# Kernel optimization log

Measured on AMD Instinct MI355X. Metric: run time of the kernel, lower is better.

The kernel has to match this reference:

```python
import jax, jax.numpy as jnp
import numpy as np

B, S, IN, H, NH = 8, 1024, 512, 512, 8
HD = H // NH
EPS = 1e-5

def _ln(x, g, b):
    m = jnp.mean(x, axis=-1, keepdims=True)
    v = jnp.mean((x - m) ** 2, axis=-1, keepdims=True)
    return (x - m) * jax.lax.rsqrt(v + EPS) * g + b

def setup_inputs() -> dict:
    key = jax.random.key(0)
    ks = iter(jax.random.split(key, 32))
    r = lambda shape: jax.random.normal(next(ks), shape, dtype=jnp.float32) * 0.02
    return {
        "x": jax.random.normal(next(ks), (B, S, IN), dtype=jnp.float32),
        "in_proj_w": r((H, IN)), "in_proj_b": jnp.zeros((H,), jnp.float32),
        "attn_qkv_w": r((3 * H, H)), "attn_qkv_b": jnp.zeros((3 * H,), jnp.float32),
        "attn_out_w": r((H, H)), "attn_out_b": jnp.zeros((H,), jnp.float32),
        "ltc_w1": r((H, 2 * H)), "ltc_b1": jnp.zeros((H,), jnp.float32),
        "ltc_w2": r((H, H)), "ltc_b2": jnp.zeros((H,), jnp.float32),
        "time_w": r((H, H)), "time_b": jnp.zeros((H,), jnp.float32),
        "g_w": r((H, H)), "g_b": jnp.zeros((H,), jnp.float32),
        "hn_w": r((H, H)), "hn_b": jnp.zeros((H,), jnp.float32),
        "norm1_g": jnp.ones((H,), jnp.float32), "norm1_b": jnp.zeros((H,), jnp.float32),
        "norm2_g": jnp.ones((H,), jnp.float32), "norm2_b": jnp.zeros((H,), jnp.float32),
        "out_w": r((IN, H)), "out_b": jnp.zeros((IN,), jnp.float32),
    }

def reference(x, in_proj_w, in_proj_b, attn_qkv_w, attn_qkv_b, attn_out_w, attn_out_b,
              ltc_w1, ltc_b1, ltc_w2, ltc_b2, time_w, time_b, g_w, g_b, hn_w, hn_b,
              norm1_g, norm1_b, norm2_g, norm2_b, out_w, out_b):
    b, s, _ = x.shape
    # input projection
    h = x @ in_proj_w.T + in_proj_b                      # [B,S,H]
    # multi-head self-attention (no mask, eval: no dropout)
    qkv = h @ attn_qkv_w.T + attn_qkv_b                  # [B,S,3H]
    q, k, v = jnp.split(qkv, 3, axis=-1)
    q = q.reshape(b, s, NH, HD)
    k = k.reshape(b, s, NH, HD)
    v = v.reshape(b, s, NH, HD)
    scores = jnp.einsum("bqhd,bkhd->bhqk", q, k) / jnp.sqrt(jnp.float32(HD))
    attn = jax.nn.softmax(scores, axis=-1)
    ctx = jnp.einsum("bhqk,bkhd->bqhd", attn, v).reshape(b, s, H)
    h_att = ctx @ attn_out_w.T + attn_out_b
    h_att = _ln(h + h_att, norm1_g, norm1_b)             # [B,S,H]
    # LTC recurrence over time via scan
    times = jnp.arange(s, dtype=jnp.float32)             # default times, same per batch
    def step(state, inp):
        xt, tt = inp                                      # [B,H], scalar
        combined = jnp.concatenate([xt, state], axis=-1)  # [B,2H]
        feats = jnp.tanh(combined @ ltc_w1.T + ltc_b1) @ ltc_w2.T + ltc_b2
        f_t = jax.nn.sigmoid(feats @ time_w.T + time_b)
        g_x = feats @ g_w.T + g_b
        h_x = feats @ hn_w.T + hn_b
        gate = jax.nn.sigmoid(-f_t * tt)
        h_new = gate * g_x + (1.0 - gate) * h_x
        return h_new, h_new
    init = jnp.zeros((b, H), x.dtype)
    _, outs = jax.lax.scan(step, init, (h_att.transpose(1, 0, 2), times))
    outs = outs.transpose(1, 0, 2)                        # [B,S,H]
    outs = _ln(outs + h_att, norm2_g, norm2_b)
    return outs @ out_w.T + out_b                         # [B,S,IN]
```

## Files before the change

kernel.cpp:

```cpp
#include <hip/hip_runtime.h>
#include <math.h>

#define HALF _Float16
typedef _Float16 half8 __attribute__((ext_vector_type(8)));
typedef float floatx4 __attribute__((ext_vector_type(4)));

#define SPIN_MAX (1 << 14)

__global__ __launch_bounds__(256) void k_cast(const float* __restrict__ s, HALF* __restrict__ d, int n) {
    int i = blockIdx.x * 256 + threadIdx.x;
    if (i < n) d[i] = (HALF)s[i];
}

__global__ __launch_bounds__(256) void k_cast_slice(const float* __restrict__ s, HALF* __restrict__ d, int off) {
    int i = blockIdx.x * 256 + threadIdx.x;
    int r = i >> 9, c = i & 511;
    d[i] = (HALF)s[r * 1024 + off + c];
}

__global__ __launch_bounds__(256) void k_transpose_cast(const float* __restrict__ s, HALF* __restrict__ d) {
    int i = blockIdx.x * 256 + threadIdx.x;
    int r = i >> 9, c = i & 511;
    d[c * 512 + r] = (HALF)s[i];
}

__global__ __launch_bounds__(256) void k_fuse_bias(const float* __restrict__ b2,
    const float* __restrict__ tw, const float* __restrict__ tb,
    const float* __restrict__ gw, const float* __restrict__ gb,
    const float* __restrict__ hw, const float* __restrict__ hb,
    float* __restrict__ bcat) {
    int i = blockIdx.x * 256 + threadIdx.x;
    if (i >= 1536) return;
    int j = i >> 9, n = i & 511;
    const float* W  = (j == 0) ? tw : (j == 1 ? gw : hw);
    const float* bb = (j == 0) ? tb : (j == 1 ? gb : hb);
    float s = bb[n];
    for (int k = 0; k < 512; ++k) s += b2[k] * W[n * 512 + k];
    bcat[i] = s;
}

__global__ __launch_bounds__(256) void k_reorderA(const float* __restrict__ in, float* __restrict__ out) {
    int i = blockIdx.x * 256 + threadIdx.x;
    int nl = i & 7, m = (i >> 3) & 7, blk = (i >> 6) & 63, t = i >> 12;
    out[i] = in[((long long)(m << 10 | t)) * 512 + blk * 8 + nl];
}

__global__ __launch_bounds__(256)
void k_gemm(const HALF* __restrict__ A, int lda, long long sAz,
            const HALF* __restrict__ Bw, int ldb, long long sBz,
            float* __restrict__ Cf, HALF* __restrict__ Ch, int ldc, long long sCz,
            const float* __restrict__ bias, float alpha,
            int M, int N, int K)
{
    __shared__ HALF As[64][72];
    __shared__ HALF Ws[64][72];
    const int tid = threadIdx.x;
    const int bx = blockIdx.x, by = blockIdx.y, z = blockIdx.z;
    A  += (long long)z * sAz;
    Bw += (long long)z * sBz;
    const long long coff = (long long)z * sCz;
    const int wave = tid >> 6, lane = tid & 63;
    const int wrow = (wave >> 1) * 32, wcol = (wave & 1) * 32;
    const int frow = lane & 15, fquad = lane >> 4;
    const int srow = tid >> 3, sch = (tid & 7) * 8;
    floatx4 acc[2][2] = {};
    for (int k0 = 0; k0 < K; k0 += 64) {
        uint4 a0 = *(const uint4*)(A + (long long)(by * 64 + srow) * lda + k0 + sch);
        uint4 a1 = *(const uint4*)(A + (long long)(by * 64 + srow + 32) * lda + k0 + sch);
        uint4 b0 = *(const uint4*)(Bw + (long long)(bx * 64 + srow) * ldb + k0 + sch);
        uint4 b1 = *(const uint4*)(Bw + (long long)(bx * 64 + srow + 32) * ldb + k0 + sch);
        *(uint4*)&As[srow][sch] = a0;
        *(uint4*)&As[srow + 32][sch] = a1;
        *(uint4*)&Ws[srow][sch] = b0;
        *(uint4*)&Ws[srow + 32][sch] = b1;
        __syncthreads();
        #pragma unroll
        for (int ks = 0; ks < 64; ks += 32) {
            half8 fa0 = *(const half8*)&As[wrow + frow][ks + fquad * 8];
            half8 fa1 = *(const half8*)&As[wrow + 16 + frow][ks + fquad * 8];
            half8 fb0 = *(const half8*)&Ws[wcol + frow][ks + fquad * 8];
            half8 fb1 = *(const half8*)&Ws[wcol + 16 + frow][ks + fquad * 8];
            acc[0][0] = __builtin_amdgcn_mfma_f32_16x16x32_f16(fa0, fb0, acc[0][0], 0, 0, 0);
            acc[0][1] = __builtin_amdgcn_mfma_f32_16x16x32_f16(fa0, fb1, acc[0][1], 0, 0, 0);
            acc[1][0] = __builtin_amdgcn_mfma_f32_16x16x32_f16(fa1, fb0, acc[1][0], 0, 0, 0);
            acc[1][1] = __builtin_amdgcn_mfma_f32_16x16x32_f16(fa1, fb1, acc[1][1], 0, 0, 0);
        }
        __syncthreads();
    }
    const int crow = (lane >> 4) * 4, ccol = lane & 15;
    #pragma unroll
    for (int i = 0; i < 2; ++i)
        #pragma unroll
        for (int j = 0; j < 2; ++j) {
            int gn = bx * 64 + wcol + j * 16 + ccol;
            float bv = bias ? bias[gn] : 0.0f;
            #pragma unroll
            for (int r = 0; r < 4; ++r) {
                int gm = by * 64 + wrow + i * 16 + crow + r;
                float v = acc[i][j][r] * alpha + bv;
                long long idx = coff + (long long)gm * ldc + gn;
                if (Cf) Cf[idx] = v;
                if (Ch) Ch[idx] = (HALF)v;
            }
        }
}

__global__ __launch_bounds__(256) void k_qkv_split(const HALF* __restrict__ qkv,
    HALF* __restrict__ Q, HALF* __restrict__ Kt, HALF* __restrict__ VT) {
    long long i = (long long)blockIdx.x * 256 + threadIdx.x;
    int c = (int)(i & 511);
    long long sg = i >> 9;
    int b = (int)(sg >> 10), s = (int)(sg & 1023);
    int h = c >> 6, d = c & 63;
    const HALF* src = qkv + sg * 1536;
    long long bh = (long long)(b * 8 + h);
    long long qi = (bh * 1024 + s) * 64 + d;
    Q[qi]  = src[c];
    Kt[qi] = src[512 + c];
    VT[(bh * 64 + d) * 1024 + s] = src[1024 + c];
}

__global__ __launch_bounds__(256) void k_softmax(HALF* __restrict__ P) {
    long long row = (long long)blockIdx.x * 4 + (threadIdx.x >> 6);
    int lane = threadIdx.x & 63;
    uint4* p = (uint4*)(P + row * 1024);
    union { uint4 u; HALF h[8]; } u0, u1;
    u0.u = p[lane * 2]; u1.u = p[lane * 2 + 1];
    float f[16];
    #pragma unroll
    for (int i = 0; i < 8; ++i) { f[i] = (float)u0.h[i]; f[8 + i] = (float)u1.h[i]; }
    float mx = f[0];
    #pragma unroll
    for (int i = 1; i < 16; ++i) mx = fmaxf(mx, f[i]);
    #pragma unroll
    for (int o = 32; o > 0; o >>= 1) mx = fmaxf(mx, __shfl_xor(mx, o, 64));
    float sm = 0.f;
    #pragma unroll
    for (int i = 0; i < 16; ++i) { f[i] = __expf(f[i] - mx); sm += f[i]; }
    #pragma unroll
    for (int o = 32; o > 0; o >>= 1) sm += __shfl_xor(sm, o, 64);
    float r = 1.0f / sm;
    #pragma unroll
    for (int i = 0; i < 8; ++i) { u0.h[i] = (HALF)(f[i] * r); u1.h[i] = (HALF)(f[8 + i] * r); }
    p[lane * 2] = u0.u; p[lane * 2 + 1] = u1.u;
}

__global__ __launch_bounds__(256) void k_ln_add(const float* __restrict__ X, const float* __restrict__ Y,
    const float* __restrict__ g, const float* __restrict__ bb,
    float* __restrict__ o32, HALF* __restrict__ o16) {
    long long row = (long long)blockIdx.x * 4 + (threadIdx.x >> 6);
    int lane = threadIdx.x & 63;
    const float4* xp = (const float4*)(X + row * 512);
    const float4* yp = (const float4*)(Y + row * 512);
    float v[8];
    float s = 0.f, s2 = 0.f;
    #pragma unroll
    for (int i = 0; i < 2; ++i) {
        float4 a = xp[lane * 2 + i], c = yp[lane * 2 + i];
        float t0 = a.x + c.x, t1 = a.y + c.y, t2 = a.z + c.z, t3 = a.w + c.w;
        v[i * 4 + 0] = t0; v[i * 4 + 1] = t1; v[i * 4 + 2] = t2; v[i * 4 + 3] = t3;
        s += t0 + t1 + t2 + t3;
        s2 += t0 * t0 + t1 * t1 + t2 * t2 + t3 * t3;
    }
    #pragma unroll
    for (int o = 32; o > 0; o >>= 1) { s += __shfl_xor(s, o, 64); s2 += __shfl_xor(s2, o, 64); }
    float mean = s * (1.0f / 512.0f);
    float var = s2 * (1.0f / 512.0f) - mean * mean;
    float rstd = rsqrtf(var + 1e-5f);
    #pragma unroll
    for (int i = 0; i < 8; ++i) {
        int c = lane * 8 + i;
        float o = (v[i] - mean) * rstd * g[c] + bb[c];
        if (o32) o32[row * 512 + c] = o;
        if (o16) o16[row * 512 + c] = (HALF)o;
    }
}

__device__ __forceinline__ floatx4 mfma16(half8 a, half8 b, floatx4 c) {
    return __builtin_amdgcn_mfma_f32_16x16x32_f16(a, b, c, 0, 0, 0);
}
__device__ __forceinline__ unsigned long long pack2h_tag(float a, float b, unsigned tag) {
    union { unsigned short u; HALF h; } x0, x1;
    x0.h = (HALF)a; x1.h = (HALF)b;
    return (unsigned long long)x0.u | ((unsigned long long)x1.u << 16)
         | ((unsigned long long)tag << 48);
}
__device__ __forceinline__ float fast_tanh(float x) {
    float e = __expf(2.0f * x);
    return 1.0f - 2.0f / (e + 1.0f);
}

__global__ __launch_bounds__(256, 1)
void k_ltc_scan(const float* __restrict__ AscanR, const HALF* __restrict__ W1hg,
                const HALF* __restrict__ Wcatg, const float* __restrict__ bcat,
                unsigned long long* __restrict__ Sbuf, unsigned long long* __restrict__ Tbuf,
                float* __restrict__ outs)
{
    __shared__ unsigned int SLu[2][2176];
    const int tid = threadIdx.x;
    const int wv = tid >> 6, lane = tid & 63;
    const int blk = blockIdx.x * 4 + wv;
    const int n0 = blk * 8;
    const int c = lane & 15, q = lane >> 4;
    const int nW = n0 + (c & 7);
    const int kq = q * 8;
    const bool valid = (q < 2) && (c < 8);
    const int pidx = blk * 16 + c * 2 + q;
    const int i0 = tid * 8;

    for (int k = tid; k < 2176; k += 256) { SLu[0][k] = 0; SLu[1][k] = 0; }

    half8 aW1[16];
    half8 aWc[3][16];
    #pragma unroll
    for (int kb = 0; kb < 16; ++kb)
        aW1[kb] = *(const half8*)(W1hg + (long long)nW * 512 + kb * 32 + kq);
    #pragma unroll
    for (int j = 0; j < 3; ++j)
        #pragma unroll
        for (int kb = 0; kb < 16; ++kb)
            aWc[j][kb] = *(const half8*)(Wcatg + ((long long)j * 512 + nW) * 512 + kb * 32 + kq);
    floatx4 binit[3];
    #pragma unroll
    for (int j = 0; j < 3; ++j) {
        float4 bv = *(const float4*)(bcat + j * 512 + n0 + (q & 1) * 4);
        binit[j][0] = bv.x; binit[j][1] = bv.y; binit[j][2] = bv.z; binit[j][3] = bv.w;
    }

    auto stage_wait = [&](const unsigned long long* __restrict__ P, unsigned tag, int p) {
        unsigned long long v[8];
        #pragma unroll
        for (int k = 0; k < 8; ++k)
            v[k] = __hip_atomic_load(P + i0 + k, __ATOMIC_RELAXED, __HIP_MEMORY_SCOPE_SYSTEM);
        int spin = 0;
        for (;;) {
            bool ok = true;
            #pragma unroll
            for (int k = 0; k < 8; ++k) ok &= ((unsigned)(v[k] >> 48) == tag);
            if (ok || ++spin > SPIN_MAX) break;
            #pragma unroll
            for (int k = 0; k < 8; ++k)
                v[k] = __hip_atomic_load(P + i0 + k, __ATOMIC_RELAXED, __HIP_MEMORY_SCOPE_SYSTEM);
        }
        #pragma unroll
        for (int k = 0; k < 8; ++k) SLu[p][i0 + k] = (unsigned)v[k];
        __syncthreads();
    };

    for (int t = 0; t < 1024; ++t) {
        float4 aval = *(const float4*)(AscanR + (long long)t * 4096 + blk * 64 + (c & 7) * 8 + (q & 1) * 4);

        stage_wait(Sbuf, (unsigned)t, 0);
        const char* SLb0 = (const char*)SLu[0];

        floatx4 c1a = {0.f, 0.f, 0.f, 0.f}, c1b = {0.f, 0.f, 0.f, 0.f};
        #pragma unroll
        for (int kb = 0; kb < 16; kb += 2) {
            half8 b0 = *(const half8*)(SLb0 + kb * 512 + q * 128 + c * 16);
            half8 b1 = *(const half8*)(SLb0 + (kb + 1) * 512 + q * 128 + c * 16);
            c1a = mfma16(aW1[kb],     b0, c1a);
            c1b = mfma16(aW1[kb + 1], b1, c1b);
        }
        floatx4 c1 = c1a + c1b;
        float tv0 = fast_tanh(c1[0] + aval.x);
        float tv1 = fast_tanh(c1[1] + aval.y);
        float tv2 = fast_tanh(c1[2] + aval.z);
        float tv3 = fast_tanh(c1[3] + aval.w);
        if (valid) {
            __hip_atomic_store(Tbuf + pidx * 2,     pack2h_tag(tv0, tv1, (unsigned)(t + 1)),
                               __ATOMIC_RELAXED, __HIP_MEMORY_SCOPE_SYSTEM);
            __hip_atomic_store(Tbuf + pidx * 2 + 1, pack2h_tag(tv2, tv3, (unsigned)(t + 1)),
                               __ATOMIC_RELAXED, __HIP_MEMORY_SCOPE_SYSTEM);
        }

        stage_wait(Tbuf, (unsigned)(t + 1), 1);
        const char* SLb1 = (const char*)SLu[1];

        floatx4 c2_0 = binit[0], c2_1 = binit[1], c2_2 = binit[2];
        #pragma unroll
        for (int kb = 0; kb < 16; ++kb) {
            half8 bT = *(const half8*)(SLb1 + kb * 512 + q * 128 + c * 16);
            c2_0 = mfma16(aWc[0][kb], bT, c2_0);
            c2_1 = mfma16(aWc[1][kb], bT, c2_1);
            c2_2 = mfma16(aWc[2][kb], bT, c2_2);
        }
        float sn[4];
        const float tf = (float)t;
        #pragma unroll
        for (int r = 0; r < 4; ++r) {
            float f = 1.0f / (1.0f + __expf(-c2_0[r]));
            float gate = 1.0f / (1.0f + __expf(f * tf));
            sn[r] = gate * c2_1[r] + (1.0f - gate) * c2_2[r];
        }
        if (valid) {
            __hip_atomic_store(Sbuf + pidx * 2,     pack2h_tag(sn[0], sn[1], (unsigned)(t + 1)),
                               __ATOMIC_RELAXED, __HIP_MEMORY_SCOPE_SYSTEM);
            __hip_atomic_store(Sbuf + pidx * 2 + 1, pack2h_tag(sn[2], sn[3], (unsigned)(t + 1)),
                               __ATOMIC_RELAXED, __HIP_MEMORY_SCOPE_SYSTEM);
            float4 ov; ov.x = sn[0]; ov.y = sn[1]; ov.z = sn[2]; ov.w = sn[3];
            *(float4*)(outs + ((long long)(c << 10 | t)) * 512 + n0 + q * 4) = ov;
        }
    }
}

extern "C" void kernel_launch(void* const* d_in, const int* in_sizes, int n_in,
                              void* d_out, int out_size, void* d_ws, size_t ws_size,
                              hipStream_t stream) {
    (void)in_sizes; (void)n_in; (void)out_size; (void)ws_size;
    const float* x       = (const float*)d_in[0];
    const float* w_in_f  = (const float*)d_in[1];
    const float* b_in    = (const float*)d_in[2];
    const float* w_qkv_f = (const float*)d_in[3];
    const float* b_qkv   = (const float*)d_in[4];
    const float* w_ao_f  = (const float*)d_in[5];
    const float* b_ao    = (const float*)d_in[6];
    const float* w1_f    = (const float*)d_in[7];
    const float* b1      = (const float*)d_in[8];
    const float* w2_f    = (const float*)d_in[9];
    const float* b2      = (const float*)d_in[10];
    const float* tw_f    = (const float*)d_in[11];
    const float* tb      = (const float*)d_in[12];
    const float* gw_f    = (const float*)d_in[13];
    const float* gb      = (const float*)d_in[14];
    const float* hw_f    = (const float*)d_in[15];
    const float* hb      = (const float*)d_in[16];
    const float* n1g     = (const float*)d_in[17];
    const float* n1b     = (const float*)d_in[18];
    const float* n2g     = (const float*)d_in[19];
    const float* n2b     = (const float*)d_in[20];
    const float* w_out_f = (const float*)d_in[21];
    const float* b_out   = (const float*)d_in[22];
    float* out = (float*)d_out;

    char* p = (char*)d_ws;
    auto alloc = [&](size_t n) { char* r = p; p += (n + 255) & ~(size_t)255; return r; };
    HALF* w_in   = (HALF*)alloc(512 * 512 * 2);
    HALF* w_qkv  = (HALF*)alloc(1536 * 512 * 2);
    HALF* w_ao   = (HALF*)alloc(512 * 512 * 2);
    HALF* w_out  = (HALF*)alloc(512 * 512 * 2);
    HALF* w_time = (HALF*)alloc(512 * 512 * 2);
    HALF* w_g    = (HALF*)alloc(512 * 512 * 2);
    HALF* w_hn   = (HALF*)alloc(512 * 512 * 2);
    HALF* W2T    = (HALF*)alloc(512 * 512 * 2);
    HALF* W1x    = (HALF*)alloc(512 * 512 * 2);
    HALF* W1h    = (HALF*)alloc(512 * 512 * 2);
    HALF* Wcat   = (HALF*)alloc(3 * 512 * 512 * 2);
    float* bcat  = (float*)alloc(3 * 512 * 4 + 64);
    HALF* xb     = (HALF*)alloc(8192ll * 512 * 2);
    float* h32   = (float*)alloc(8192ll * 512 * 4);
    HALF* h16    = (HALF*)alloc(8192ll * 512 * 2);
    HALF* qkv16  = (HALF*)alloc(8192ll * 1536 * 2);
    HALF* Q16    = (HALF*)alloc(8192ll * 512 * 2);
    HALF* K16    = (HALF*)alloc(8192ll * 512 * 2);
    HALF* VT16   = (HALF*)alloc(8192ll * 512 * 2);
    HALF* P16    = (HALF*)alloc(8ll * 1024 * 1024 * 2);
    unsigned long long* Sbuf = (unsigned long long*)alloc(16384 + 256);
    unsigned long long* Tbuf = (unsigned long long*)alloc(16384 + 256);

    HALF*  ctx16      = xb;
    float* attnproj32 = (float*)qkv16;
    float* hatt32     = (float*)P16;
    HALF*  hatt16     = VT16;
    float* Ascan32    = h32;
    float* AscanR     = (float*)K16;
    float* outs32     = (float*)qkv16;
    HALF*  y16        = h16;

    hipMemsetAsync(Sbuf, 0, (16384 + 256) * 2, stream);

    k_cast<<<1024, 256, 0, stream>>>(w_in_f, w_in, 262144);
    k_cast<<<3072, 256, 0, stream>>>(w_qkv_f, w_qkv, 786432);
    k_cast<<<1024, 256, 0, stream>>>(w_ao_f, w_ao, 262144);
    k_cast<<<1024, 256, 0, stream>>>(w_out_f, w_out, 262144);
    k_cast<<<1024, 256, 0, stream>>>(tw_f, w_time, 262144);
    k_cast<<<1024, 256, 0, stream>>>(gw_f, w_g, 262144);
    k_cast<<<1024, 256, 0, stream>>>(hw_f, w_hn, 262144);
    k_cast<<<16384, 256, 0, stream>>>(x, xb, 4194304);
    k_transpose_cast<<<1024, 256, 0, stream>>>(w2_f, W2T);
    k_cast_slice<<<1024, 256, 0, stream>>>(w1_f, W1x, 0);
    k_cast_slice<<<1024, 256, 0, stream>>>(w1_f, W1h, 512);
    k_fuse_bias<<<6, 256, 0, stream>>>(b2, tw_f, tb, gw_f, gb, hw_f, hb, bcat);

    dim3 g88(8, 8, 1);
    k_gemm<<<g88, 256, 0, stream>>>(w_time, 512, 0, W2T, 512, 0, nullptr, Wcat,          512, 0, nullptr, 1.0f, 512, 512, 512);
    k_gemm<<<g88, 256, 0, stream>>>(w_g,    512, 0, W2T, 512, 0, nullptr, Wcat + 262144, 512, 0, nullptr, 1.0f, 512, 512, 512);
    k_gemm<<<g88, 256, 0, stream>>>(w_hn,   512, 0, W2T, 512, 0, nullptr, Wcat + 524288, 512, 0, nullptr, 1.0f, 512, 512, 512);

    dim3 gh(8, 128, 1);
    k_gemm<<<gh, 256, 0, stream>>>(xb, 512, 0, w_in, 512, 0, h32, h16, 512, 0, b_in, 1.0f, 8192, 512, 512);
    dim3 gq(24, 128, 1);
    k_gemm<<<gq, 256, 0, stream>>>(h16, 512, 0, w_qkv, 512, 0, nullptr, qkv16, 1536, 0, b_qkv, 1.0f, 8192, 1536, 512);
    k_qkv_split<<<16384, 256, 0, stream>>>(qkv16, Q16, K16, VT16);

    for (int c = 0; c < 8; ++c) {
        dim3 gs(16, 16, 8);
        k_gemm<<<gs, 256, 0, stream>>>(Q16 + c * 524288, 64, 65536, K16 + c * 524288, 64, 65536,
                                       nullptr, P16, 1024, 1048576, nullptr, 0.125f, 1024, 1024, 64);
        k_softmax<<<2048, 256, 0, stream>>>(P16);
        dim3 gc(1, 16, 8);
        k_gemm<<<gc, 256, 0, stream>>>(P16, 1024, 1048576, VT16 + c * 524288, 1024, 65536,
                                       nullptr, ctx16 + (long long)c * 524288, 512, 64, nullptr, 1.0f, 1024, 64, 1024);
    }

    k_gemm<<<gh, 256, 0, stream>>>(ctx16, 512, 0, w_ao, 512, 0, attnproj32, nullptr, 512, 0, b_ao, 1.0f, 8192, 512, 512);
    k_ln_add<<<2048, 256, 0, stream>>>(h32, attnproj32, n1g, n1b, hatt32, hatt16);

    k_gemm<<<gh, 256, 0, stream>>>(hatt16, 512, 0, W1x, 512, 0, Ascan32, nullptr, 512, 0, b1, 1.0f, 8192, 512, 512);
    k_reorderA<<<16384, 256, 0, stream>>>(Ascan32, AscanR);

    k_ltc_scan<<<16, 256, 0, stream>>>(AscanR, W1h, Wcat, bcat, Sbuf, Tbuf, outs32);

    k_ln_add<<<2048, 256, 0, stream>>>(outs32, hatt32, n2g, n2b, nullptr, y16);
    k_gemm<<<gh, 256, 0, stream>>>(y16, 512, 0, w_out, 512, 0, out, nullptr, 512, 0, b_out, 1.0f, 8192, 512, 512);
}
```

Before: 6.055 ms.

## Give each wave a private LDS state copy and drop block-wide barriers in scan

```diff
diff --git a/kernel.cpp b/kernel.cpp
--- a/kernel.cpp
+++ b/kernel.cpp
@@ -196,7 +196,7 @@
                 unsigned long long* __restrict__ Sbuf, unsigned long long* __restrict__ Tbuf,
                 float* __restrict__ outs)
 {
-    __shared__ unsigned int SLu[2][2176];
+    __shared__ unsigned int SLu[2][4][2176];
     const int tid = threadIdx.x;
     const int wv = tid >> 6, lane = tid & 63;
     const int blk = blockIdx.x * 4 + wv;
@@ -206,9 +206,8 @@
     const int kq = q * 8;
     const bool valid = (q < 2) && (c < 8);
     const int pidx = blk * 16 + c * 2 + q;
-    const int i0 = tid * 8;
-
-    for (int k = tid; k < 2176; k += 256) { SLu[0][k] = 0; SLu[1][k] = 0; }
+
+    for (int k = lane; k < 2176; k += 64) { SLu[0][wv][k] = 0; SLu[1][wv][k] = 0; }
 
     half8 aW1[16];
     half8 aWc[3][16];
@@ -226,32 +225,43 @@
         float4 bv = *(const float4*)(bcat + j * 512 + n0 + (q & 1) * 4);
         binit[j][0] = bv.x; binit[j][1] = bv.y; binit[j][2] = bv.z; binit[j][3] = bv.w;
     }
-
-    auto stage_wait = [&](const unsigned long long* __restrict__ P, unsigned tag, int p) {
-        unsigned long long v[8];
-        #pragma unroll
-        for (int k = 0; k < 8; ++k)
-            v[k] = __hip_atomic_load(P + i0 + k, __ATOMIC_RELAXED, __HIP_MEMORY_SCOPE_SYSTEM);
-        int spin = 0;
-        for (;;) {
-            bool ok = true;
+    #pragma unroll
+    for (int kb = 0; kb < 16; ++kb) asm volatile("" : "+v"(aW1[kb]));
+    #pragma unroll
+    for (int j = 0; j < 3; ++j)
+        #pragma unroll
+        for (int kb = 0; kb < 16; ++kb) asm volatile("" : "+v"(aWc[j][kb]));
+    #pragma unroll
+    for (int j = 0; j < 3; ++j) asm volatile("" : "+v"(binit[j]));
+
+    auto stage_wait = [&](const unsigned long long* __restrict__ P, unsigned tag, unsigned int* __restrict__ SL) {
+        #pragma unroll
+        for (int ch = 0; ch < 4; ++ch) {
+            const int base = lane + ch * 512;
+            unsigned long long v[8];
             #pragma unroll
-            for (int k = 0; k < 8; ++k) ok &= ((unsigned)(v[k] >> 48) == tag);
-            if (ok || ++spin > SPIN_MAX) break;
+            for (int j = 0; j < 8; ++j)
+                v[j] = __hip_atomic_load(P + base + 64 * j, __ATOMIC_RELAXED, __HIP_MEMORY_SCOPE_SYSTEM);
+            int spin = 0;
+            for (;;) {
+                bool ok = true;
+                #pragma unroll
+                for (int j = 0; j < 8; ++j) ok &= ((unsigned)(v[j] >> 48) == tag);
+                if (ok || ++spin > SPIN_MAX) break;
+                #pragma unroll
+                for (int j = 0; j < 8; ++j)
+                    v[j] = __hip_atomic_load(P + base + 64 * j, __ATOMIC_RELAXED, __HIP_MEMORY_SCOPE_SYSTEM);
+            }
             #pragma unroll
-            for (int k = 0; k < 8; ++k)
-                v[k] = __hip_atomic_load(P + i0 + k, __ATOMIC_RELAXED, __HIP_MEMORY_SCOPE_SYSTEM);
-        }
-        #pragma unroll
-        for (int k = 0; k < 8; ++k) SLu[p][i0 + k] = (unsigned)v[k];
-        __syncthreads();
+            for (int j = 0; j < 8; ++j) SL[base + 64 * j] = (unsigned)v[j];
+        }
     };
 
     for (int t = 0; t < 1024; ++t) {
         float4 aval = *(const float4*)(AscanR + (long long)t * 4096 + blk * 64 + (c & 7) * 8 + (q & 1) * 4);
 
-        stage_wait(Sbuf, (unsigned)t, 0);
-        const char* SLb0 = (const char*)SLu[0];
+        stage_wait(Sbuf, (unsigned)t, SLu[0][wv]);
+        const char* SLb0 = (const char*)SLu[0][wv];
 
         floatx4 c1a = {0.f, 0.f, 0.f, 0.f}, c1b = {0.f, 0.f, 0.f, 0.f};
         #pragma unroll
@@ -273,8 +283,8 @@
                                __ATOMIC_RELAXED, __HIP_MEMORY_SCOPE_SYSTEM);
         }
 
-        stage_wait(Tbuf, (unsigned)(t + 1), 1);
-        const char* SLb1 = (const char*)SLu[1];
+        stage_wait(Tbuf, (unsigned)(t + 1), SLu[1][wv]);
+        const char* SLb1 = (const char*)SLu[1][wv];
 
         floatx4 c2_0 = binit[0], c2_1 = binit[1], c2_2 = binit[2];
         #pragma unroll
```

New measurement: 8.722 ms. +44.0%, slower.

## Halve LTC scan workgroups by giving each wave 16 output columns

Applied to the files above, without the earlier changes.

```diff
diff --git a/kernel.cpp b/kernel.cpp
--- a/kernel.cpp
+++ b/kernel.cpp
@@ -199,13 +199,11 @@
     __shared__ unsigned int SLu[2][2176];
     const int tid = threadIdx.x;
     const int wv = tid >> 6, lane = tid & 63;
-    const int blk = blockIdx.x * 4 + wv;
-    const int n0 = blk * 8;
+    const int slice = blockIdx.x * 4 + wv;
+    const int n0 = slice * 16;
     const int c = lane & 15, q = lane >> 4;
-    const int nW = n0 + (c & 7);
-    const int kq = q * 8;
-    const bool valid = (q < 2) && (c < 8);
-    const int pidx = blk * 16 + c * 2 + q;
+    const bool valid = (c < 8);
+    const int w0 = slice * 64 + c * 8 + q * 2;
     const int i0 = tid * 8;
 
     for (int k = tid; k < 2176; k += 256) { SLu[0][k] = 0; SLu[1][k] = 0; }
@@ -214,16 +212,16 @@
     half8 aWc[3][16];
     #pragma unroll
     for (int kb = 0; kb < 16; ++kb)
-        aW1[kb] = *(const half8*)(W1hg + (long long)nW * 512 + kb * 32 + kq);
+        aW1[kb] = *(const half8*)(W1hg + (long long)(n0 + c) * 512 + kb * 32 + q * 8);
     #pragma unroll
     for (int j = 0; j < 3; ++j)
         #pragma unroll
         for (int kb = 0; kb < 16; ++kb)
-            aWc[j][kb] = *(const half8*)(Wcatg + ((long long)j * 512 + nW) * 512 + kb * 32 + kq);
+            aWc[j][kb] = *(const half8*)(Wcatg + ((long long)j * 512 + n0 + c) * 512 + kb * 32 + q * 8);
     floatx4 binit[3];
     #pragma unroll
     for (int j = 0; j < 3; ++j) {
-        float4 bv = *(const float4*)(bcat + j * 512 + n0 + (q & 1) * 4);
+        float4 bv = *(const float4*)(bcat + j * 512 + n0 + q * 4);
         binit[j][0] = bv.x; binit[j][1] = bv.y; binit[j][2] = bv.z; binit[j][3] = bv.w;
     }
 
@@ -248,7 +246,8 @@
     };
 
     for (int t = 0; t < 1024; ++t) {
-        float4 aval = *(const float4*)(AscanR + (long long)t * 4096 + blk * 64 + (c & 7) * 8 + (q & 1) * 4);
+        float4 aval = *(const float4*)(AscanR + (long long)t * 4096
+                                       + slice * 128 + (q >> 1) * 64 + c * 8 + (q & 1) * 4);
 
         stage_wait(Sbuf, (unsigned)t, 0);
         const char* SLb0 = (const char*)SLu[0];
@@ -256,8 +255,8 @@
         floatx4 c1a = {0.f, 0.f, 0.f, 0.f}, c1b = {0.f, 0.f, 0.f, 0.f};
         #pragma unroll
         for (int kb = 0; kb < 16; kb += 2) {
-            half8 b0 = *(const half8*)(SLb0 + kb * 512 + q * 128 + c * 16);
-            half8 b1 = *(const half8*)(SLb0 + (kb + 1) * 512 + q * 128 + c * 16);
+            half8 b0 = *(const half8*)(SLb0 + kb * 512 + (q >> 1) * 256 + c * 32 + (q & 1) * 16);
+            half8 b1 = *(const half8*)(SLb0 + (kb + 1) * 512 + (q >> 1) * 256 + c * 32 + (q & 1) * 16);
             c1a = mfma16(aW1[kb],     b0, c1a);
             c1b = mfma16(aW1[kb + 1], b1, c1b);
         }
@@ -267,9 +266,9 @@
         float tv2 = fast_tanh(c1[2] + aval.z);
         float tv3 = fast_tanh(c1[3] + aval.w);
         if (valid) {
-            __hip_atomic_store(Tbuf + pidx * 2,     pack2h_tag(tv0, tv1, (unsigned)(t + 1)),
+            __hip_atomic_store(Tbuf + w0,     pack2h_tag(tv0, tv1, (unsigned)(t + 1)),
                                __ATOMIC_RELAXED, __HIP_MEMORY_SCOPE_SYSTEM);
-            __hip_atomic_store(Tbuf + pidx * 2 + 1, pack2h_tag(tv2, tv3, (unsigned)(t + 1)),
+            __hip_atomic_store(Tbuf + w0 + 1, pack2h_tag(tv2, tv3, (unsigned)(t + 1)),
                                __ATOMIC_RELAXED, __HIP_MEMORY_SCOPE_SYSTEM);
         }
 
@@ -279,7 +278,7 @@
         floatx4 c2_0 = binit[0], c2_1 = binit[1], c2_2 = binit[2];
         #pragma unroll
         for (int kb = 0; kb < 16; ++kb) {
-            half8 bT = *(const half8*)(SLb1 + kb * 512 + q * 128 + c * 16);
+            half8 bT = *(const half8*)(SLb1 + kb * 512 + (q >> 1) * 256 + c * 32 + (q & 1) * 16);
             c2_0 = mfma16(aWc[0][kb], bT, c2_0);
             c2_1 = mfma16(aWc[1][kb], bT, c2_1);
             c2_2 = mfma16(aWc[2][kb], bT, c2_2);
@@ -293,9 +292,9 @@
             sn[r] = gate * c2_1[r] + (1.0f - gate) * c2_2[r];
         }
         if (valid) {
-            __hip_atomic_store(Sbuf + pidx * 2,     pack2h_tag(sn[0], sn[1], (unsigned)(t + 1)),
+            __hip_atomic_store(Sbuf + w0,     pack2h_tag(sn[0], sn[1], (unsigned)(t + 1)),
                                __ATOMIC_RELAXED, __HIP_MEMORY_SCOPE_SYSTEM);
-            __hip_atomic_store(Sbuf + pidx * 2 + 1, pack2h_tag(sn[2], sn[3], (unsigned)(t + 1)),
+            __hip_atomic_store(Sbuf + w0 + 1, pack2h_tag(sn[2], sn[3], (unsigned)(t + 1)),
                                __ATOMIC_RELAXED, __HIP_MEMORY_SCOPE_SYSTEM);
             float4 ov; ov.x = sn[0]; ov.y = sn[1]; ov.z = sn[2]; ov.w = sn[3];
             *(float4*)(outs + ((long long)(c << 10 | t)) * 512 + n0 + q * 4) = ov;
@@ -408,7 +407,7 @@
     k_gemm<<<gh, 256, 0, stream>>>(hatt16, 512, 0, W1x, 512, 0, Ascan32, nullptr, 512, 0, b1, 1.0f, 8192, 512, 512);
     k_reorderA<<<16384, 256, 0, stream>>>(Ascan32, AscanR);
 
-    k_ltc_scan<<<16, 256, 0, stream>>>(AscanR, W1h, Wcat, bcat, Sbuf, Tbuf, outs32);
+    k_ltc_scan<<<8, 256, 0, stream>>>(AscanR, W1h, Wcat, bcat, Sbuf, Tbuf, outs32);
 
     k_ln_add<<<2048, 256, 0, stream>>>(outs32, hatt32, n2g, n2b, nullptr, y16);
     k_gemm<<<gh, 256, 0, stream>>>(y16, 512, 0, w_out, 512, 0, out, nullptr, 512, 0, b_out, 1.0f, 8192, 512, 512);
```

After: 5.854 ms, median of 2. 3.3% less time.
